# Performance work log

Measured on AMD Instinct MI355X. Metric: run time of the kernel, lower is better.

The kernel has to match this reference:

```python
import jax, jax.numpy as jnp
import numpy as np

B, N, C, D = 8, 16384, 256, 32
EPS = 1e-6


def setup_inputs() -> dict:
    key = jax.random.key(0)
    ks = jax.random.split(key, 16)
    g = lambda k, shape, s=0.05: jax.random.normal(k, shape, dtype=jnp.float32) * s
    inp = {
        "x": g(ks[0], (B, N, C), 1.0),
        "y": g(ks[1], (B, N, C), 1.0),
        "Wq": g(ks[2], (D, C)), "bq": g(ks[3], (D,), 0.01),
        "Wk": g(ks[4], (D, C)), "bk": g(ks[5], (D,), 0.01),
        "Wv": g(ks[6], (C, C)), "bv": g(ks[7], (C,), 0.01),
        "Wqy": g(ks[8], (D, C)), "bqy": g(ks[9], (D,), 0.01),
        "Wky": g(ks[10], (D, C)), "bky": g(ks[11], (D,), 0.01),
        "Wvy": g(ks[12], (C, C)), "bvy": g(ks[13], (C,), 0.01),
        # gammas are nn.Parameter(torch.zeros(1)); random-init so outputs/grads are nontrivial
        "gamma": jnp.full((1,), 0.7, jnp.float32),
        "gamma_y": jnp.full((1,), 0.6, jnp.float32),
        "gamma_cx": jnp.full((1,), 0.5, jnp.float32),
        "gamma_cy": jnp.full((1,), 0.4, jnp.float32),
        "wx1": jnp.float32(0.5), "wx2": jnp.float32(0.5),
        "wy1": jnp.float32(0.5), "wy2": jnp.float32(0.5),
    }
    return inp


def _conv1x1(t, W, b):
    # t: [b,c,n]; 1x1 Conv2d == per-position linear
    return jnp.einsum('oc,bcn->bon', W, t) + b[None, :, None]


def _l2norm(t):
    # torch l2_norm: divide each spatial column by its channel-dim L2 norm
    return t / jnp.linalg.norm(t, axis=-2, keepdims=True)


def _branch(Qt, Ksum, mat, vsum, n):
    # Qt:[b,n,d]  Ksum:[b,d]  mat=K@V^T:[b,d,c]  vsum:[b,c]
    tailor = 1.0 / (n + jnp.einsum('bnd,bd->bn', Qt, Ksum))      # [b,n]
    msum = vsum[:, :, None] + jnp.einsum('bnd,bdc->bcn', Qt, mat)  # [b,c,n]
    return msum * tailor[:, None, :]


def reference(x, y, Wq, bq, Wk, bk, Wv, bv, Wqy, bqy, Wky, bky, Wvy, bvy,
              gamma, gamma_y, gamma_cx, gamma_cy, wx1, wx2, wy1, wy2):
    b, n, c = x.shape
    xb = jnp.transpose(x, (0, 2, 1))  # [b,c,n]
    yb = jnp.transpose(y, (0, 2, 1))
    Q = _l2norm(_conv1x1(xb, Wq, bq))      # [b,d,n]
    K = _l2norm(_conv1x1(xb, Wk, bk))
    V = _conv1x1(xb, Wv, bv)               # [b,c,n]
    Qy = _l2norm(_conv1x1(yb, Wqy, bqy))
    Ky = _l2norm(_conv1x1(yb, Wky, bky))
    Vy = _conv1x1(yb, Wvy, bvy)
    Qt = jnp.transpose(Q, (0, 2, 1))       # [b,n,d]
    Qyt = jnp.transpose(Qy, (0, 2, 1))
    Ksum = K.sum(-1) + EPS                 # [b,d]
    Kysum = Ky.sum(-1) + EPS
    vsum = V.sum(-1)                       # [b,c]
    vysum = Vy.sum(-1)
    mat = jnp.einsum('bdn,bcn->bdc', K, V)     # [b,d,c]
    maty = jnp.einsum('bdn,bcn->bdc', Ky, Vy)
    att = gamma * _branch(Qt, Ksum, mat, vsum, n)          # self x
    atty = gamma_y * _branch(Qyt, Kysum, maty, vysum, n)   # self y
    att_cx = gamma_cx * _branch(Qt, Kysum, maty, vsum, n)  # cross x<-y
    att_cy = gamma_cy * _branch(Qyt, Ksum, mat, vysum, n)  # cross y<-x
    fx = jnp.transpose(att * wx1 + att_cx * wx2, (0, 2, 1))  # [b,n,c]
    fy = jnp.transpose(atty * wy1 + att_cy * wy2, (0, 2, 1))
    return (fx, fy)
```

## Files before the change

kernel.cpp:

```cpp
#include <hip/hip_runtime.h>

#define BB 8
#define NN 16384
#define CC 256
#define DD 32
#define EPSF 1e-6f

#define QBUF_FLOATS (2ull*BB*NN*DD)
#define ACC_STRIDE 8480
#define ACC_OFF QBUF_FLOATS
#define ACC_FLOATS (16*ACC_STRIDE)
#define FIN_OFF (ACC_OFF + ACC_FLOATS)
#define FIN_STRIDE 8480
#define WBF_OFF (FIN_OFF + 16*FIN_STRIDE)
#define MATT_OFF (WBF_OFF + 16384)

typedef __attribute__((ext_vector_type(8))) short bh8;
typedef __attribute__((ext_vector_type(4))) float f4;
typedef __attribute__((ext_vector_type(2))) unsigned int u32x2;

__device__ __forceinline__ unsigned int bfp(float f) {
    unsigned int u = __float_as_uint(f);
    return (u + 0x7FFFu + ((u >> 16) & 1u)) >> 16;
}
__device__ __forceinline__ float bf2f(unsigned int h) {
    return __uint_as_float(h << 16);
}

#define MFMA16 __builtin_amdgcn_mfma_f32_16x16x32_bf16

#define LBAR() do { \
    asm volatile("s_waitcnt lgkmcnt(0)" ::: "memory"); \
    __builtin_amdgcn_s_barrier(); \
    __builtin_amdgcn_sched_barrier(0); \
} while (0)

__global__ __launch_bounds__(256)
void k0_cvt(const float* __restrict__ Wk, const float* __restrict__ Wq,
            const float* __restrict__ Wky, const float* __restrict__ Wqy,
            unsigned short* __restrict__ wbf)
{
    int i = blockIdx.x * 256 + threadIdx.x;
    const float* p = (i < 8192) ? Wk : (i < 16384) ? Wq : (i < 24576) ? Wky : Wqy;
    wbf[i] = (unsigned short)bfp(p[i & 8191]);
}

__global__ __launch_bounds__(256, 2)
void k1_proj(const float* __restrict__ x, const float* __restrict__ y,
             const unsigned short* __restrict__ wbf,
             const float* __restrict__ bk, const float* __restrict__ bq,
             const float* __restrict__ bky, const float* __restrict__ bqy,
             unsigned short* __restrict__ qbuf16, float* __restrict__ acc,
             float* __restrict__ pbuf)
{
    const int b = blockIdx.y, s = blockIdx.z;
    const float* __restrict__ src = (s ? y : x) + (size_t)b * NN * CC;
    unsigned short* __restrict__ qb = qbuf16 + (size_t)(s*BB + b) * NN * DD;
    float* __restrict__ accsb = acc + (size_t)(s*BB + b) * ACC_STRIDE;
    float* __restrict__ pout = pbuf + ((size_t)((s*BB + b) * 64 + blockIdx.x)) * 8192;

    __shared__ unsigned short Xsub[2][8192];
    __shared__ unsigned short Ksb[1024];
    __shared__ float red[4][32];
    __shared__ float xred[4][256];

    const int tid = threadIdx.x;
    const int w = tid >> 6, lane = tid & 63;
    const int l15 = lane & 15, l4 = lane >> 4;
    const int oct = lane & 31;
    const int rower = tid >> 5;

    const unsigned short* __restrict__ wm =
        wbf + (size_t)(s * 2 + (w >> 1)) * 8192 + (size_t)(16 * (w & 1) + l15) * 256 + 8 * l4;
    bh8 wf[8];
    #pragma unroll
    for (int ks = 0; ks < 8; ++ks) wf[ks] = *(const bh8*)(wm + 32 * ks);
    const float* __restrict__ bp = (w < 2) ? (s ? bky : bk) : (s ? bqy : bq);
    const f4 bias4 = *(const f4*)(bp + 16 * (w & 1) + 4 * l4);

    const int hv = (rower >> 2) & 1;
    const int wbyte0 = (hv * 2048 + (oct >> 1) * 128 + (rower & 3) * 32 + (oct & 1) * 16) ^ (hv << 4);
    int ab[2];
    #pragma unroll
    for (int pt = 0; pt < 2; ++pt) {
        int aq = 4 * pt + (l15 >> 2);
        ab[pt] = ((aq * 2048 + (l15 & 3) * 32 + (l4 & 1) * 16) ^ ((aq & 1) << 4)) + (l4 >> 1) * 128;
    }
    const unsigned xb0 = (unsigned)(uintptr_t)&Xsub[0][0];
    const unsigned kbase = (unsigned)(uintptr_t)&Ksb[0];
    const unsigned btr_rel = (unsigned)(2 * l4 * 2048 + 4 * w * 128 + l15 * 8);
    const unsigned atr = kbase + (unsigned)(2 * l4 * 256 + l15 * 8);

    f4 g2[2][4];
    #pragma unroll
    for (int dt = 0; dt < 2; ++dt)
        #pragma unroll
        for (int ct = 0; ct < 4; ++ct) g2[dt][ct] = (f4){0.f, 0.f, 0.f, 0.f};
    float xs[8];
    #pragma unroll
    for (int j = 0; j < 8; ++j) xs[j] = 0.f;
    float kreg[4] = {0.f, 0.f, 0.f, 0.f};

    const float* __restrict__ gbase = src + (size_t)(blockIdx.x * 256 + rower) * CC + oct * 8;

    auto do_chunk = [&](char* xcur, unsigned kb, int ch) {
        LBAR();
        f4 a1_0 = bias4, a1_1 = bias4;
        #pragma unroll
        for (int ks = 0; ks < 8; ++ks) {
            bh8 xv0 = *(const bh8*)(xcur + ab[0] + ks * 256);
            bh8 xv1 = *(const bh8*)(xcur + ab[1] + ks * 256);
            a1_0 = MFMA16(wf[ks], xv0, a1_0, 0, 0, 0);
            a1_1 = MFMA16(wf[ks], xv1, a1_1, 0, 0, 0);
        }
        {
            float s0 = a1_0[0]*a1_0[0] + a1_0[1]*a1_0[1] + a1_0[2]*a1_0[2] + a1_0[3]*a1_0[3];
            float s1 = a1_1[0]*a1_1[0] + a1_1[1]*a1_1[1] + a1_1[2]*a1_1[2] + a1_1[3]*a1_1[3];
            s0 += __shfl_xor(s0, 16); s0 += __shfl_xor(s0, 32);
            s1 += __shfl_xor(s1, 16); s1 += __shfl_xor(s1, 32);
            if (l4 == 0) { red[w][l15] = s0; red[w][16 + l15] = s1; }
        }
        LBAR();
        if (w < 2) {
            {
                int p = l15;
                float n = rsqrtf(red[0][p] + red[1][p]);
                float k0 = a1_0[0]*n, k1 = a1_0[1]*n, k2 = a1_0[2]*n, k3 = a1_0[3]*n;
                kreg[0] += k0; kreg[1] += k1; kreg[2] += k2; kreg[3] += k3;
                *(uint2*)((char*)Ksb + (p >> 2) * 256 + (w & 1) * 128 + (p & 3) * 32 + 8 * l4)
                    = make_uint2(bfp(k0) | (bfp(k1) << 16), bfp(k2) | (bfp(k3) << 16));
            }
            {
                int p = 16 + l15;
                float n = rsqrtf(red[0][p] + red[1][p]);
                float k0 = a1_1[0]*n, k1 = a1_1[1]*n, k2 = a1_1[2]*n, k3 = a1_1[3]*n;
                kreg[0] += k0; kreg[1] += k1; kreg[2] += k2; kreg[3] += k3;
                *(uint2*)((char*)Ksb + (p >> 2) * 256 + (w & 1) * 128 + (p & 3) * 32 + 8 * l4)
                    = make_uint2(bfp(k0) | (bfp(k1) << 16), bfp(k2) | (bfp(k3) << 16));
            }
        } else {
            {
                int p = l15;
                float n = rsqrtf(red[2][p] + red[3][p]);
                *(uint2*)(qb + (size_t)(blockIdx.x*256 + ch*32 + p) * DD + 16 * (w & 1) + 4 * l4)
                    = make_uint2(bfp(a1_0[0]*n) | (bfp(a1_0[1]*n) << 16),
                                 bfp(a1_0[2]*n) | (bfp(a1_0[3]*n) << 16));
            }
            {
                int p = 16 + l15;
                float n = rsqrtf(red[2][p] + red[3][p]);
                *(uint2*)(qb + (size_t)(blockIdx.x*256 + ch*32 + p) * DD + 16 * (w & 1) + 4 * l4)
                    = make_uint2(bfp(a1_1[0]*n) | (bfp(a1_1[1]*n) << 16),
                                 bfp(a1_1[2]*n) | (bfp(a1_1[3]*n) << 16));
            }
        }
        LBAR();
        u32x2 ta0, ta1, ta2, ta3, tb0, tb1, tb2, tb3, tb4, tb5, tb6, tb7;
        asm volatile("ds_read_b64_tr_b16 %0, %1" : "=v"(ta0) : "v"(atr));
        asm volatile("ds_read_b64_tr_b16 %0, %1" : "=v"(ta1) : "v"(atr + 256u));
        asm volatile("ds_read_b64_tr_b16 %0, %1" : "=v"(ta2) : "v"(atr + 128u));
        asm volatile("ds_read_b64_tr_b16 %0, %1" : "=v"(ta3) : "v"(atr + 384u));
        asm volatile("ds_read_b64_tr_b16 %0, %1" : "=v"(tb0) : "v"(kb));
        asm volatile("ds_read_b64_tr_b16 %0, %1" : "=v"(tb1) : "v"((kb + 2048u) ^ 16u));
        asm volatile("ds_read_b64_tr_b16 %0, %1" : "=v"(tb2) : "v"(kb + 128u));
        asm volatile("ds_read_b64_tr_b16 %0, %1" : "=v"(tb3) : "v"((kb + 2176u) ^ 16u));
        asm volatile("ds_read_b64_tr_b16 %0, %1" : "=v"(tb4) : "v"(kb + 256u));
        asm volatile("ds_read_b64_tr_b16 %0, %1" : "=v"(tb5) : "v"((kb + 2304u) ^ 16u));
        asm volatile("ds_read_b64_tr_b16 %0, %1" : "=v"(tb6) : "v"(kb + 384u));
        asm volatile("ds_read_b64_tr_b16 %0, %1" : "=v"(tb7) : "v"((kb + 2432u) ^ 16u));
        asm volatile("s_waitcnt lgkmcnt(8)" ::: "memory");
        __builtin_amdgcn_sched_barrier(0);
        union { unsigned u[4]; bh8 v; } A0, A1;
        A0.u[0] = ta0[0]; A0.u[1] = ta0[1]; A0.u[2] = ta1[0]; A0.u[3] = ta1[1];
        A1.u[0] = ta2[0]; A1.u[1] = ta2[1]; A1.u[2] = ta3[0]; A1.u[3] = ta3[1];
        asm volatile("s_waitcnt lgkmcnt(6)" ::: "memory");
        __builtin_amdgcn_sched_barrier(0);
        {
            union { unsigned u[4]; bh8 v; } Bc;
            Bc.u[0] = tb0[0]; Bc.u[1] = tb0[1]; Bc.u[2] = tb1[0]; Bc.u[3] = tb1[1];
            g2[0][0] = MFMA16(A0.v, Bc.v, g2[0][0], 0, 0, 0);
            g2[1][0] = MFMA16(A1.v, Bc.v, g2[1][0], 0, 0, 0);
        }
        asm volatile("s_waitcnt lgkmcnt(4)" ::: "memory");
        __builtin_amdgcn_sched_barrier(0);
        {
            union { unsigned u[4]; bh8 v; } Bc;
            Bc.u[0] = tb2[0]; Bc.u[1] = tb2[1]; Bc.u[2] = tb3[0]; Bc.u[3] = tb3[1];
            g2[0][1] = MFMA16(A0.v, Bc.v, g2[0][1], 0, 0, 0);
            g2[1][1] = MFMA16(A1.v, Bc.v, g2[1][1], 0, 0, 0);
        }
        asm volatile("s_waitcnt lgkmcnt(2)" ::: "memory");
        __builtin_amdgcn_sched_barrier(0);
        {
            union { unsigned u[4]; bh8 v; } Bc;
            Bc.u[0] = tb4[0]; Bc.u[1] = tb4[1]; Bc.u[2] = tb5[0]; Bc.u[3] = tb5[1];
            g2[0][2] = MFMA16(A0.v, Bc.v, g2[0][2], 0, 0, 0);
            g2[1][2] = MFMA16(A1.v, Bc.v, g2[1][2], 0, 0, 0);
        }
        asm volatile("s_waitcnt lgkmcnt(0)" ::: "memory");
        __builtin_amdgcn_sched_barrier(0);
        {
            union { unsigned u[4]; bh8 v; } Bc;
            Bc.u[0] = tb6[0]; Bc.u[1] = tb6[1]; Bc.u[2] = tb7[0]; Bc.u[3] = tb7[1];
            g2[0][3] = MFMA16(A0.v, Bc.v, g2[0][3], 0, 0, 0);
            g2[1][3] = MFMA16(A1.v, Bc.v, g2[1][3], 0, 0, 0);
        }
    };

#define LOADSET(R0,R1,R2,R3,R4,R5,R6,R7, CHIX) do { \
    const float* gn_ = gbase + (size_t)((CHIX) * 32) * CC; \
    R0 = *(const float4*)(gn_);              R1 = *(const float4*)(gn_ + 4); \
    R2 = *(const float4*)(gn_ +  8*CC);      R3 = *(const float4*)(gn_ +  8*CC + 4); \
    R4 = *(const float4*)(gn_ + 16*CC);      R5 = *(const float4*)(gn_ + 16*CC + 4); \
    R6 = *(const float4*)(gn_ + 24*CC);      R7 = *(const float4*)(gn_ + 24*CC + 4); \
} while (0)

#define PACK1(Av, Bv, XCUR, ITOFF) do { \
    xs[0] += Av.x; xs[1] += Av.y; xs[2] += Av.z; xs[3] += Av.w; \
    xs[4] += Bv.x; xs[5] += Bv.y; xs[6] += Bv.z; xs[7] += Bv.w; \
    uint4 pk_; \
    pk_.x = bfp(Av.x) | (bfp(Av.y) << 16); \
    pk_.y = bfp(Av.z) | (bfp(Av.w) << 16); \
    pk_.z = bfp(Bv.x) | (bfp(Bv.y) << 16); \
    pk_.w = bfp(Bv.z) | (bfp(Bv.w) << 16); \
    *(uint4*)((XCUR) + wbyte0 + (ITOFF)) = pk_; \
} while (0)

#define CONSUME(R0,R1,R2,R3,R4,R5,R6,R7, XCUR) do { \
    PACK1(R0, R1, XCUR, 0); \
    PACK1(R2, R3, XCUR, 4096); \
    PACK1(R4, R5, XCUR, 8192); \
    PACK1(R6, R7, XCUR, 12288); \
} while (0)

    float4 A0,A1,A2,A3,A4,A5,A6,A7;
    float4 C0,C1,C2,C3,C4,C5,C6,C7;

    LOADSET(A0,A1,A2,A3,A4,A5,A6,A7, 0);
    LOADSET(C0,C1,C2,C3,C4,C5,C6,C7, 1);

    char* xbuf0 = (char*)&Xsub[0][0];
    char* xbuf1 = (char*)&Xsub[1][0];

    for (int it2 = 0; it2 < 4; ++it2) {
        const int che = 2 * it2, cho = che + 1;
        CONSUME(A0,A1,A2,A3,A4,A5,A6,A7, xbuf0);
        if (it2 < 3) LOADSET(A0,A1,A2,A3,A4,A5,A6,A7, che + 2);
        do_chunk(xbuf0, xb0 + btr_rel, che);
        CONSUME(C0,C1,C2,C3,C4,C5,C6,C7, xbuf1);
        if (it2 < 3) LOADSET(C0,C1,C2,C3,C4,C5,C6,C7, cho + 2);
        do_chunk(xbuf1, xb0 + 16384u + btr_rel, cho);
    }
#undef LOADSET
#undef PACK1
#undef CONSUME

    #pragma unroll
    for (int dt = 0; dt < 2; ++dt)
        #pragma unroll
        for (int ct = 0; ct < 4; ++ct)
            #pragma unroll
            for (int r = 0; r < 4; ++r)
                pout[(16 * dt + 4 * l4 + r) * 256 + 64 * w + 16 * ct + l15] = g2[dt][ct][r];

    #pragma unroll
    for (int j = 0; j < 8; ++j) xs[j] += __shfl_xor(xs[j], 32);
    if ((lane >> 5) == 0) {
        #pragma unroll
        for (int j = 0; j < 8; ++j) xred[w][oct * 8 + j] = xs[j];
    }
    __syncthreads();
    {
        float v = xred[0][tid] + xred[1][tid] + xred[2][tid] + xred[3][tid];
        atomicAdd(accsb + 8192 + tid, v);
    }
    if (w < 2) {
        #pragma unroll
        for (int r = 0; r < 4; ++r) {
            float v = kreg[r];
            v += __shfl_xor(v, 1); v += __shfl_xor(v, 2);
            v += __shfl_xor(v, 4); v += __shfl_xor(v, 8);
            if (l15 == 0) atomicAdd(accsb + 8448 + 16 * (w & 1) + 4 * l4 + r, v);
        }
    }
}

__global__ __launch_bounds__(256)
void k2a_reduce(const float* __restrict__ pbuf, float* __restrict__ acc)
{
    const int b = blockIdx.x, s = blockIdx.y, cs = blockIdx.z;
    const float* __restrict__ p = pbuf + (size_t)(s*BB + b) * 64 * 8192;
    float* __restrict__ a = acc + (size_t)(s*BB + b) * ACC_STRIDE;
    const int d = threadIdx.x >> 3, c = cs * 32 + (threadIdx.x & 7) * 4;
    f4 v = (f4){0.f, 0.f, 0.f, 0.f};
    for (int j = 0; j < 64; ++j)
        v += *(const f4*)(p + (size_t)j * 8192 + d * 256 + c);
    *(f4*)(a + d * 256 + c) = v;
}

__global__ __launch_bounds__(256, 2)
void k2_finalize(const float* __restrict__ Wv, const float* __restrict__ bv,
                 const float* __restrict__ Wvy, const float* __restrict__ bvy,
                 const float* __restrict__ acc, float* __restrict__ fin,
                 unsigned short* __restrict__ matT)
{
    const int b = blockIdx.x, s = blockIdx.y;
    const float* __restrict__ Wv_ = s ? Wvy : Wv;
    const float* __restrict__ bv_ = s ? bvy : bv;
    const float* __restrict__ a = acc + (size_t)(s*BB + b) * ACC_STRIDE;
    float* __restrict__ f = fin + (size_t)(s*BB + b) * FIN_STRIDE;
    unsigned short* __restrict__ mt = matT + (size_t)b * 16384;

    __shared__ float KXt[256][36];
    __shared__ float xsh[256];
    __shared__ float ks0[32];

    const int tid = threadIdx.x;
    for (int d = 0; d < 32; ++d) KXt[tid][d] = a[d*256 + tid];
    xsh[tid] = a[8192 + tid];
    if (tid < 32) { float v = a[8448 + tid]; ks0[tid] = v; f[8448 + tid] = v + EPSF; }
    __syncthreads();

    const int dh = tid >> 7;
    const int c0 = (tid & 127) * 2;
    float macc[16][2];
    #pragma unroll
    for (int i = 0; i < 16; ++i) { macc[i][0]=0.f; macc[i][1]=0.f; }
    float v0 = 0.f, v1 = 0.f;

    for (int k4 = 0; k4 < 256; k4 += 4) {
        float4 wa = *(const float4*)(Wv_ + (size_t)c0*256 + k4);
        float4 wb = *(const float4*)(Wv_ + (size_t)(c0+1)*256 + k4);
        float4 xv = *(const float4*)&xsh[k4];
        v0 += wa.x*xv.x + wa.y*xv.y + wa.z*xv.z + wa.w*xv.w;
        v1 += wb.x*xv.x + wb.y*xv.y + wb.z*xv.z + wb.w*xv.w;
        #pragma unroll
        for (int u = 0; u < 4; ++u) {
            float wau = (u==0)?wa.x:(u==1)?wa.y:(u==2)?wa.z:wa.w;
            float wbu = (u==0)?wb.x:(u==1)?wb.y:(u==2)?wb.z:wb.w;
            #pragma unroll
            for (int i4 = 0; i4 < 16; i4 += 4) {
                float4 kxv = *(const float4*)&KXt[k4+u][dh*16 + i4];
                macc[i4+0][0] += kxv.x*wau; macc[i4+0][1] += kxv.x*wbu;
                macc[i4+1][0] += kxv.y*wau; macc[i4+1][1] += kxv.y*wbu;
                macc[i4+2][0] += kxv.z*wau; macc[i4+2][1] += kxv.z*wbu;
                macc[i4+3][0] += kxv.w*wau; macc[i4+3][1] += kxv.w*wbu;
            }
        }
    }
    float bvc0 = bv_[c0], bvc1 = bv_[c0+1];
    if (dh == 0) {
        f[8192 + c0]     = v0 + (float)NN * bvc0;
        f[8192 + c0 + 1] = v1 + (float)NN * bvc1;
    }
    union { unsigned short h[16]; uint4 q[2]; } r0u, r1u;
    #pragma unroll
    for (int i = 0; i < 16; ++i) {
        int d = dh*16 + i;
        float m0v = macc[i][0] + ks0[d]*bvc0;
        float m1v = macc[i][1] + ks0[d]*bvc1;
        f[d*256 + c0]     = m0v;
        f[d*256 + c0 + 1] = m1v;
        r0u.h[i] = (unsigned short)bfp(m0v);
        r1u.h[i] = (unsigned short)bfp(m1v);
    }
    const int kk = s * 32 + dh * 16;
    *(uint4*)(mt + (size_t)c0 * 64 + kk)           = r0u.q[0];
    *(uint4*)(mt + (size_t)c0 * 64 + kk + 8)       = r0u.q[1];
    *(uint4*)(mt + (size_t)(c0+1) * 64 + kk)       = r1u.q[0];
    *(uint4*)(mt + (size_t)(c0+1) * 64 + kk + 8)   = r1u.q[1];
}

__global__ __launch_bounds__(256, 3)
void k3_output(const unsigned short* __restrict__ qbuf16, const float* __restrict__ fin,
               const unsigned short* __restrict__ matT,
               const float* __restrict__ g_gamma, const float* __restrict__ g_gammay,
               const float* __restrict__ g_gammacx, const float* __restrict__ g_gammacy,
               const float* __restrict__ g_wx1, const float* __restrict__ g_wx2,
               const float* __restrict__ g_wy1, const float* __restrict__ g_wy2,
               float* __restrict__ out)
{
    const int b = blockIdx.y;
    const int p0 = blockIdx.x * 32;
    const float* __restrict__ fx_ = fin + (size_t)(0*BB + b) * FIN_STRIDE;
    const float* __restrict__ fy_ = fin + (size_t)(1*BB + b) * FIN_STRIDE;
    const unsigned short* __restrict__ mb = matT + (size_t)b * 16384;

    __shared__ unsigned short Msb[256 * 64];
    __shared__ unsigned short Atb[64 * 64];
    __shared__ float vs[2][256];
    __shared__ float sv[64];
    __shared__ float ksl[2][32];

    const int tid = threadIdx.x;
    if (tid < 64) ksl[tid >> 5][tid & 31] = ((tid < 32) ? fx_ : fy_)[8448 + (tid & 31)];
    vs[0][tid] = fx_[8192 + tid];
    vs[1][tid] = fy_[8192 + tid];

    #pragma unroll
    for (int i = 0; i < 8; ++i) {
        int c = (tid >> 3) + i * 32;
        int g8 = tid & 7;
        uint4 v = *(const uint4*)(mb + (size_t)c * 64 + g8 * 8);
        unsigned off = (unsigned)(c * 128 + g8 * 16) ^ (unsigned)((c & 7) << 4);
        *(uint4*)((char*)Msb + off) = v;
    }
    __syncthreads();

    if (tid < 64) {
        const int str = tid >> 5;
        const int p = p0 + (tid & 31);
        const uint4* __restrict__ qp = (const uint4*)(qbuf16 + ((size_t)(str*BB + b) * NN + p) * DD);
        float q[32];
        float ss = 0.f;
        #pragma unroll
        for (int m = 0; m < 4; ++m) {
            uint4 u = qp[m];
            unsigned uu[4] = {u.x, u.y, u.z, u.w};
            #pragma unroll
            for (int j = 0; j < 4; ++j) {
                float lo = bf2f(uu[j] & 0xFFFFu), hi = bf2f(uu[j] >> 16);
                q[m*8 + 2*j] = lo; q[m*8 + 2*j + 1] = hi;
                ss += lo*lo + hi*hi;
            }
        }
        float qn = rsqrtf(ss);
        float dK = 0.f, dKy = 0.f;
        #pragma unroll
        for (int d = 0; d < 32; ++d) { dK += q[d]*ksl[0][d]; dKy += q[d]*ksl[1][d]; }
        dK *= qn; dKy *= qn;
        float clo, chi, svr;
        if (str == 0) {
            float t1 = 1.f / ((float)NN + dK);
            float t2 = 1.f / ((float)NN + dKy);
            float a1c = g_gamma[0]   * g_wx1[0] * t1;
            float a2c = g_gammacx[0] * g_wx2[0] * t2;
            clo = a1c * qn; chi = a2c * qn; svr = a1c + a2c;
        } else {
            float ty1 = 1.f / ((float)NN + dKy);
            float ty2 = 1.f / ((float)NN + dK);
            float b1c = g_gammay[0]  * g_wy1[0] * ty1;
            float b2c = g_gammacy[0] * g_wy2[0] * ty2;
            clo = b2c * qn; chi = b1c * qn; svr = b1c + b2c;
        }
        sv[tid] = svr;
        #pragma unroll
        for (int g = 0; g < 8; ++g) {
            float m0 = (g < 4) ? clo : chi;
            const float* qq = q + (g & 3) * 8;
            uint4 pk;
            pk.x = bfp(m0*qq[0]) | (bfp(m0*qq[1]) << 16);
            pk.y = bfp(m0*qq[2]) | (bfp(m0*qq[3]) << 16);
            pk.z = bfp(m0*qq[4]) | (bfp(m0*qq[5]) << 16);
            pk.w = bfp(m0*qq[6]) | (bfp(m0*qq[7]) << 16);
            unsigned off = (unsigned)(tid * 128 + g * 16) ^ (unsigned)((tid & 7) << 4);
            *(uint4*)((char*)Atb + off) = pk;
        }
    }
    __syncthreads();

    const int w = tid >> 6, lane = tid & 63;
    const int l15 = lane & 15, l4 = lane >> 4;
    const int r = w * 16 + l15;
    f4 accv[16];
    #pragma unroll
    for (int ct = 0; ct < 16; ++ct) accv[ct] = (f4){0.f, 0.f, 0.f, 0.f};

    #pragma unroll
    for (int kstep = 0; kstep < 2; ++kstep) {
        unsigned boff = (unsigned)(r * 128 + kstep * 64 + l4 * 16) ^ (unsigned)((r & 7) << 4);
        bh8 bfr = *(const bh8*)((const char*)Atb + boff);
        #pragma unroll
        for (int ct = 0; ct < 16; ++ct) {
            int c = ct * 16 + l15;
            unsigned aoff = (unsigned)(c * 128 + kstep * 64 + l4 * 16) ^ (unsigned)((c & 7) << 4);
            bh8 afr = *(const bh8*)((const char*)Msb + aoff);
            accv[ct] = MFMA16(afr, bfr, accv[ct], 0, 0, 0);
        }
    }

    const int str = w >> 1;
    const int prow = (w & 1) * 16 + l15;
    float* __restrict__ op = out + (size_t)str * BB * NN * CC + ((size_t)b * NN + p0 + prow) * CC;
    const float svr = sv[r];
    #pragma unroll
    for (int ct = 0; ct < 16; ++ct) {
        int c0 = ct * 16 + 4 * l4;
        float4 vsv = *(const float4*)&vs[str][c0];
        float4 o = make_float4(accv[ct][0] + svr*vsv.x, accv[ct][1] + svr*vsv.y,
                               accv[ct][2] + svr*vsv.z, accv[ct][3] + svr*vsv.w);
        *(float4*)(op + c0) = o;
    }
}

extern "C" void kernel_launch(void* const* d_in, const int* in_sizes, int n_in,
                              void* d_out, int out_size, void* d_ws, size_t ws_size,
                              hipStream_t stream)
{
    (void)in_sizes; (void)n_in; (void)out_size; (void)ws_size;
    const float* x   = (const float*)d_in[0];
    const float* y   = (const float*)d_in[1];
    const float* Wq  = (const float*)d_in[2];
    const float* bq  = (const float*)d_in[3];
    const float* Wk  = (const float*)d_in[4];
    const float* bk  = (const float*)d_in[5];
    const float* Wv  = (const float*)d_in[6];
    const float* bv  = (const float*)d_in[7];
    const float* Wqy = (const float*)d_in[8];
    const float* bqy = (const float*)d_in[9];
    const float* Wky = (const float*)d_in[10];
    const float* bky = (const float*)d_in[11];
    const float* Wvy = (const float*)d_in[12];
    const float* bvy = (const float*)d_in[13];

    float* ws   = (float*)d_ws;
    unsigned short* qbuf16 = (unsigned short*)ws;
    float* acc  = ws + ACC_OFF;
    float* fin  = ws + FIN_OFF;
    unsigned short* wbf  = (unsigned short*)(ws + WBF_OFF);
    unsigned short* matT = (unsigned short*)(ws + MATT_OFF);
    float* pbuf = (float*)d_out;

    k0_cvt<<<128, 256, 0, stream>>>(Wk, Wq, Wky, Wqy, wbf);
    hipMemsetAsync(acc, 0, ACC_FLOATS * sizeof(float), stream);

    k1_proj<<<dim3(64, BB, 2), 256, 0, stream>>>(x, y, wbf, bk, bq, bky, bqy, qbuf16, acc, pbuf);
    k2a_reduce<<<dim3(BB, 2, 8), 256, 0, stream>>>(pbuf, acc);
    k2_finalize<<<dim3(BB, 2), 256, 0, stream>>>(Wv, bv, Wvy, bvy, acc, fin, matT);
    k3_output<<<dim3(NN/32, BB), 256, 0, stream>>>(qbuf16, fin, matT,
        (const float*)d_in[14], (const float*)d_in[15], (const float*)d_in[16], (const float*)d_in[17],
        (const float*)d_in[18], (const float*)d_in[19], (const float*)d_in[20], (const float*)d_in[21],
        (float*)d_out);
}
```

Baseline: 198.4 us.

## Repartition projection MFMA so each wave owns full D, removing LDS norm reduction

```diff
diff --git a/kernel.cpp b/kernel.cpp
--- a/kernel.cpp
+++ b/kernel.cpp
@@ -61,7 +61,6 @@
 
     __shared__ unsigned short Xsub[2][8192];
     __shared__ unsigned short Ksb[1024];
-    __shared__ float red[4][32];
     __shared__ float xred[4][256];
 
     const int tid = threadIdx.x;
@@ -69,23 +68,23 @@
     const int l15 = lane & 15, l4 = lane >> 4;
     const int oct = lane & 31;
     const int rower = tid >> 5;
-
-    const unsigned short* __restrict__ wm =
-        wbf + (size_t)(s * 2 + (w >> 1)) * 8192 + (size_t)(16 * (w & 1) + l15) * 256 + 8 * l4;
-    bh8 wf[8];
-    #pragma unroll
-    for (int ks = 0; ks < 8; ++ks) wf[ks] = *(const bh8*)(wm + 32 * ks);
+    const int phalf = w & 1;
+
+    const unsigned short* __restrict__ wmat = wbf + (size_t)(s * 2 + (w >> 1)) * 8192;
+    bh8 wlo[8], whi[8];
+    #pragma unroll
+    for (int ks = 0; ks < 8; ++ks) {
+        wlo[ks] = *(const bh8*)(wmat + (size_t)l15 * 256 + 32 * ks + 8 * l4);
+        whi[ks] = *(const bh8*)(wmat + (size_t)(16 + l15) * 256 + 32 * ks + 8 * l4);
+    }
     const float* __restrict__ bp = (w < 2) ? (s ? bky : bk) : (s ? bqy : bq);
-    const f4 bias4 = *(const f4*)(bp + 16 * (w & 1) + 4 * l4);
+    const f4 bias_lo = *(const f4*)(bp + 4 * l4);
+    const f4 bias_hi = *(const f4*)(bp + 16 + 4 * l4);
 
     const int hv = (rower >> 2) & 1;
     const int wbyte0 = (hv * 2048 + (oct >> 1) * 128 + (rower & 3) * 32 + (oct & 1) * 16) ^ (hv << 4);
-    int ab[2];
-    #pragma unroll
-    for (int pt = 0; pt < 2; ++pt) {
-        int aq = 4 * pt + (l15 >> 2);
-        ab[pt] = ((aq * 2048 + (l15 & 3) * 32 + (l4 & 1) * 16) ^ ((aq & 1) << 4)) + (l4 >> 1) * 128;
-    }
+    const int aq = 4 * phalf + (l15 >> 2);
+    const int abx = ((aq * 2048 + (l15 & 3) * 32 + (l4 & 1) * 16) ^ ((aq & 1) << 4)) + (l4 >> 1) * 128;
     const unsigned xb0 = (unsigned)(uintptr_t)&Xsub[0][0];
     const unsigned kbase = (unsigned)(uintptr_t)&Ksb[0];
     const unsigned btr_rel = (unsigned)(2 * l4 * 2048 + 4 * w * 128 + l15 * 8);
@@ -99,60 +98,43 @@
     float xs[8];
     #pragma unroll
     for (int j = 0; j < 8; ++j) xs[j] = 0.f;
-    float kreg[4] = {0.f, 0.f, 0.f, 0.f};
+    float kregl[4] = {0.f, 0.f, 0.f, 0.f};
+    float kregh[4] = {0.f, 0.f, 0.f, 0.f};
 
     const float* __restrict__ gbase = src + (size_t)(blockIdx.x * 256 + rower) * CC + oct * 8;
 
     auto do_chunk = [&](char* xcur, unsigned kb, int ch) {
         LBAR();
-        f4 a1_0 = bias4, a1_1 = bias4;
+        f4 a1_0 = bias_lo, a1_1 = bias_hi;
         #pragma unroll
         for (int ks = 0; ks < 8; ++ks) {
-            bh8 xv0 = *(const bh8*)(xcur + ab[0] + ks * 256);
-            bh8 xv1 = *(const bh8*)(xcur + ab[1] + ks * 256);
-            a1_0 = MFMA16(wf[ks], xv0, a1_0, 0, 0, 0);
-            a1_1 = MFMA16(wf[ks], xv1, a1_1, 0, 0, 0);
-        }
-        {
-            float s0 = a1_0[0]*a1_0[0] + a1_0[1]*a1_0[1] + a1_0[2]*a1_0[2] + a1_0[3]*a1_0[3];
-            float s1 = a1_1[0]*a1_1[0] + a1_1[1]*a1_1[1] + a1_1[2]*a1_1[2] + a1_1[3]*a1_1[3];
-            s0 += __shfl_xor(s0, 16); s0 += __shfl_xor(s0, 32);
-            s1 += __shfl_xor(s1, 16); s1 += __shfl_xor(s1, 32);
-            if (l4 == 0) { red[w][l15] = s0; red[w][16 + l15] = s1; }
-        }
-        LBAR();
+            bh8 xbv = *(const bh8*)(xcur + abx + ks * 256);
+            a1_0 = MFMA16(wlo[ks], xbv, a1_0, 0, 0, 0);
+            a1_1 = MFMA16(whi[ks], xbv, a1_1, 0, 0, 0);
+        }
+        float ss = a1_0[0]*a1_0[0] + a1_0[1]*a1_0[1] + a1_0[2]*a1_0[2] + a1_0[3]*a1_0[3]
+                 + a1_1[0]*a1_1[0] + a1_1[1]*a1_1[1] + a1_1[2]*a1_1[2] + a1_1[3]*a1_1[3];
+        ss += __shfl_xor(ss, 16);
+        ss += __shfl_xor(ss, 32);
+        const float n = rsqrtf(ss);
+        const int p = 16 * phalf + l15;
         if (w < 2) {
-            {
-                int p = l15;
-                float n = rsqrtf(red[0][p] + red[1][p]);
-                float k0 = a1_0[0]*n, k1 = a1_0[1]*n, k2 = a1_0[2]*n, k3 = a1_0[3]*n;
-                kreg[0] += k0; kreg[1] += k1; kreg[2] += k2; kreg[3] += k3;
-                *(uint2*)((char*)Ksb + (p >> 2) * 256 + (w & 1) * 128 + (p & 3) * 32 + 8 * l4)
-                    = make_uint2(bfp(k0) | (bfp(k1) << 16), bfp(k2) | (bfp(k3) << 16));
-            }
-            {
-                int p = 16 + l15;
-                float n = rsqrtf(red[0][p] + red[1][p]);
-                float k0 = a1_1[0]*n, k1 = a1_1[1]*n, k2 = a1_1[2]*n, k3 = a1_1[3]*n;
-                kreg[0] += k0; kreg[1] += k1; kreg[2] += k2; kreg[3] += k3;
-                *(uint2*)((char*)Ksb + (p >> 2) * 256 + (w & 1) * 128 + (p & 3) * 32 + 8 * l4)
-                    = make_uint2(bfp(k0) | (bfp(k1) << 16), bfp(k2) | (bfp(k3) << 16));
-            }
+            float k0 = a1_0[0]*n, k1 = a1_0[1]*n, k2 = a1_0[2]*n, k3 = a1_0[3]*n;
+            kregl[0] += k0; kregl[1] += k1; kregl[2] += k2; kregl[3] += k3;
+            *(uint2*)((char*)Ksb + (p >> 2) * 256 + (p & 3) * 32 + 8 * l4)
+                = make_uint2(bfp(k0) | (bfp(k1) << 16), bfp(k2) | (bfp(k3) << 16));
+            float h0 = a1_1[0]*n, h1 = a1_1[1]*n, h2 = a1_1[2]*n, h3 = a1_1[3]*n;
+            kregh[0] += h0; kregh[1] += h1; kregh[2] += h2; kregh[3] += h3;
+            *(uint2*)((char*)Ksb + (p >> 2) * 256 + 128 + (p & 3) * 32 + 8 * l4)
+                = make_uint2(bfp(h0) | (bfp(h1) << 16), bfp(h2) | (bfp(h3) << 16));
         } else {
-            {
-                int p = l15;
-                float n = rsqrtf(red[2][p] + red[3][p]);
-                *(uint2*)(qb + (size_t)(blockIdx.x*256 + ch*32 + p) * DD + 16 * (w & 1) + 4 * l4)
-                    = make_uint2(bfp(a1_0[0]*n) | (bfp(a1_0[1]*n) << 16),
-                                 bfp(a1_0[2]*n) | (bfp(a1_0[3]*n) << 16));
-            }
-            {
-                int p = 16 + l15;
-                float n = rsqrtf(red[2][p] + red[3][p]);
-                *(uint2*)(qb + (size_t)(blockIdx.x*256 + ch*32 + p) * DD + 16 * (w & 1) + 4 * l4)
-                    = make_uint2(bfp(a1_1[0]*n) | (bfp(a1_1[1]*n) << 16),
-                                 bfp(a1_1[2]*n) | (bfp(a1_1[3]*n) << 16));
-            }
+            unsigned short* qp = qb + (size_t)(blockIdx.x * 256 + ch * 32 + p) * DD;
+            *(uint2*)(qp + 4 * l4)
+                = make_uint2(bfp(a1_0[0]*n) | (bfp(a1_0[1]*n) << 16),
+                             bfp(a1_0[2]*n) | (bfp(a1_0[3]*n) << 16));
+            *(uint2*)(qp + 16 + 4 * l4)
+                = make_uint2(bfp(a1_1[0]*n) | (bfp(a1_1[1]*n) << 16),
+                             bfp(a1_1[2]*n) | (bfp(a1_1[3]*n) << 16));
         }
         LBAR();
         u32x2 ta0, ta1, ta2, ta3, tb0, tb1, tb2, tb3, tb4, tb5, tb6, tb7;
@@ -245,11 +227,11 @@
     for (int it2 = 0; it2 < 4; ++it2) {
         const int che = 2 * it2, cho = che + 1;
         CONSUME(A0,A1,A2,A3,A4,A5,A6,A7, xbuf0);
+        do_chunk(xbuf0, xb0 + btr_rel, che);
         if (it2 < 3) LOADSET(A0,A1,A2,A3,A4,A5,A6,A7, che + 2);
-        do_chunk(xbuf0, xb0 + btr_rel, che);
         CONSUME(C0,C1,C2,C3,C4,C5,C6,C7, xbuf1);
+        do_chunk(xbuf1, xb0 + 16384u + btr_rel, cho);
         if (it2 < 3) LOADSET(C0,C1,C2,C3,C4,C5,C6,C7, cho + 2);
-        do_chunk(xbuf1, xb0 + 16384u + btr_rel, cho);
     }
 #undef LOADSET
 #undef PACK1
@@ -277,10 +259,17 @@
     if (w < 2) {
         #pragma unroll
         for (int r = 0; r < 4; ++r) {
-            float v = kreg[r];
+            float v = kregl[r];
             v += __shfl_xor(v, 1); v += __shfl_xor(v, 2);
             v += __shfl_xor(v, 4); v += __shfl_xor(v, 8);
-            if (l15 == 0) atomicAdd(accsb + 8448 + 16 * (w & 1) + 4 * l4 + r, v);
+            if (l15 == 0) atomicAdd(accsb + 8448 + 4 * l4 + r, v);
+        }
+        #pragma unroll
+        for (int r = 0; r < 4; ++r) {
+            float v = kregh[r];
+            v += __shfl_xor(v, 1); v += __shfl_xor(v, 2);
+            v += __shfl_xor(v, 4); v += __shfl_xor(v, 8);
+            if (l15 == 0) atomicAdd(accsb + 8448 + 16 + 4 * l4 + r, v);
         }
     }
 }
```

Result: slower. 221.8 us (+11.8%).
